# Optimization experiments

Hardware: AMD Instinct MI355X
Metric: run time of the kernel (lower is better)

Reference implementation:

```python
import jax, jax.numpy as jnp
import numpy as np

B, N, M = 262144, 8, 4  # batch, state dim, measurement dim


def _tril_square(x, n):
    """x: (b, n(n+1)/2) linearized lower-tri elems -> L @ L.T, (b, n, n)."""
    i, j = np.tril_indices(n)
    L = jnp.zeros((x.shape[0], n, n), dtype=x.dtype).at[:, i, j].set(x)
    return jnp.einsum('bik,bjk->bij', L, L)


def setup_inputs() -> dict:
    key = jax.random.key(0)
    ks = jax.random.split(key, 7)
    measurement = jax.random.normal(ks[0], (B, M), dtype=jnp.float32)
    state = jax.random.normal(ks[1], (B, N), dtype=jnp.float32)
    # SPD state covariance: A A^T / n + I
    A = jax.random.normal(ks[2], (B, N, N), dtype=jnp.float32) * 0.3
    state_cov = jnp.einsum('bik,bjk->bij', A, A) / N + jnp.eye(N, dtype=jnp.float32)
    F = jnp.eye(N, dtype=jnp.float32) + 0.1 * jax.random.normal(ks[3], (B, N, N), dtype=jnp.float32)
    H = jax.random.normal(ks[4], (B, M, N), dtype=jnp.float32) * 0.5
    process_noise = jax.random.normal(ks[5], (B, N * (N + 1) // 2), dtype=jnp.float32) * 0.1
    measurement_noise = jax.random.normal(ks[6], (B, M * (M + 1) // 2), dtype=jnp.float32) * 0.3
    return {
        'measurement': measurement, 'state': state, 'state_cov': state_cov,
        'F': F, 'H': H,
        'process_noise': process_noise, 'measurement_noise': measurement_noise,
    }


def reference(measurement, state, state_cov, F, H, process_noise, measurement_noise):
    b, n = state.shape
    m = measurement.shape[1]
    Q = _tril_square(process_noise, n)       # (b, n, n) process noise cov
    R = _tril_square(measurement_noise, m)   # (b, m, m) measurement noise cov

    # Predict
    new_state = jnp.einsum('bij,bj->bi', F, state)
    new_state_cov = jnp.einsum('bij,bjk,blk->bil', F, state_cov, F) + Q

    # Update
    prediction = jnp.einsum('bij,bj->bi', H, new_state)
    res = measurement - prediction
    res_cov = jnp.einsum('bij,bjk,blk->bil', H, new_state_cov, H) + R  # (b, m, m)
    PHt = jnp.einsum('bij,bkj->bik', new_state_cov, H)                 # (b, n, m)
    kgain = jnp.matmul(PHt, jnp.linalg.inv(res_cov))                   # (b, n, m)

    upd_state = new_state + jnp.einsum('bij,bj->bi', kgain, res)
    I = jnp.eye(n, dtype=state.dtype)
    upd_cov = jnp.matmul(I - jnp.matmul(kgain, H), new_state_cov)
    return prediction, upd_state, upd_cov
```

## Files before the change

kernel.cpp:

```cpp
#include <hip/hip_runtime.h>

#define DEVINL __device__ __forceinline__

#define TIX(i, j) ((i) * ((i) + 1) / 2 + (j))
#define SYM(arr, i, j) ((i) >= (j) ? arr[TIX(i, j)] : arr[TIX(j, i)])

DEVINL void inv4(const float* m, float* inv) {
    float s0 = m[0] * m[5] - m[1] * m[4];
    float s1 = m[0] * m[6] - m[2] * m[4];
    float s2 = m[0] * m[7] - m[3] * m[4];
    float s3 = m[1] * m[6] - m[2] * m[5];
    float s4 = m[1] * m[7] - m[3] * m[5];
    float s5 = m[2] * m[7] - m[3] * m[6];
    float c5 = m[10] * m[15] - m[11] * m[14];
    float c4 = m[9] * m[15] - m[11] * m[13];
    float c3 = m[9] * m[14] - m[10] * m[13];
    float c2 = m[8] * m[15] - m[11] * m[12];
    float c1 = m[8] * m[14] - m[10] * m[12];
    float c0 = m[8] * m[13] - m[9] * m[12];
    float det = s0 * c5 - s1 * c4 + s2 * c3 + s3 * c2 - s4 * c1 + s5 * c0;
    float id = 1.0f / det;
    inv[0]  = ( m[5] * c5 - m[6] * c4 + m[7] * c3) * id;
    inv[1]  = (-m[1] * c5 + m[2] * c4 - m[3] * c3) * id;
    inv[2]  = ( m[13] * s5 - m[14] * s4 + m[15] * s3) * id;
    inv[3]  = (-m[9] * s5 + m[10] * s4 - m[11] * s3) * id;
    inv[4]  = (-m[4] * c5 + m[6] * c2 - m[7] * c1) * id;
    inv[5]  = ( m[0] * c5 - m[2] * c2 + m[3] * c1) * id;
    inv[6]  = (-m[12] * s5 + m[14] * s2 - m[15] * s1) * id;
    inv[7]  = ( m[8] * s5 - m[10] * s2 + m[11] * s1) * id;
    inv[8]  = ( m[4] * c4 - m[5] * c2 + m[7] * c0) * id;
    inv[9]  = (-m[0] * c4 + m[1] * c2 - m[3] * c0) * id;
    inv[10] = ( m[12] * s4 - m[13] * s2 + m[15] * s0) * id;
    inv[11] = (-m[8] * s4 + m[9] * s2 - m[11] * s0) * id;
    inv[12] = (-m[4] * c3 + m[5] * c1 - m[6] * c0) * id;
    inv[13] = ( m[0] * c3 - m[1] * c1 + m[2] * c0) * id;
    inv[14] = (-m[12] * s3 + m[13] * s1 - m[14] * s0) * id;
    inv[15] = ( m[8] * s3 - m[9] * s1 + m[10] * s0) * id;
}

__global__ __launch_bounds__(256) void ekf_kernel(
    const float* __restrict__ meas,
    const float* __restrict__ state,
    const float* __restrict__ Pin,
    const float* __restrict__ Fin,
    const float* __restrict__ Hin,
    const float* __restrict__ pnin,
    const float* __restrict__ mnin,
    float* __restrict__ out_pred,
    float* __restrict__ out_state,
    float* __restrict__ out_cov)
{
    const int t  = threadIdx.x;
    const int bb = blockIdx.x * 256;
    const int b  = bb + t;

    __shared__ float4 buf[2304];

    {
        const float4* g = reinterpret_cast<const float4*>(pnin) + (size_t)bb * 9;
        #pragma unroll
        for (int i = 0; i < 9; ++i) buf[i * 256 + t] = g[i * 256 + t];
    }
    __syncthreads();
    float Pn[36];
    {
        float Lq[36];
        #pragma unroll
        for (int q = 0; q < 9; ++q) {
            float4 v = buf[t * 9 + q];
            Lq[4 * q] = v.x; Lq[4 * q + 1] = v.y; Lq[4 * q + 2] = v.z; Lq[4 * q + 3] = v.w;
        }
        #pragma unroll
        for (int i = 0; i < 8; ++i)
            #pragma unroll
            for (int j = 0; j <= i; ++j) {
                float acc = 0.f;
                #pragma unroll
                for (int k = 0; k <= j; ++k)
                    acc += Lq[TIX(i, k)] * Lq[TIX(j, k)];
                Pn[TIX(i, j)] = acc;
            }
    }
    __syncthreads();

    {
        const float4* g = reinterpret_cast<const float4*>(state) + (size_t)bb * 2;
        #pragma unroll
        for (int i = 0; i < 2; ++i) {
            int f = i * 256 + t;
            buf[(f >> 1) * 3 + (f & 1)] = g[f];
        }
    }
    __syncthreads();
    float s[8];
    {
        float4 a = buf[t * 3 + 0], c = buf[t * 3 + 1];
        s[0] = a.x; s[1] = a.y; s[2] = a.z; s[3] = a.w;
        s[4] = c.x; s[5] = c.y; s[6] = c.z; s[7] = c.w;
    }
    __syncthreads();

    float Ps[36];
    #pragma unroll
    for (int h = 0; h < 2; ++h) {
        {
            const float4* g = reinterpret_cast<const float4*>(Pin) + (size_t)bb * 16;
            #pragma unroll
            for (int i = 0; i < 8; ++i) {
                int fl = i * 256 + t;
                int bq = fl >> 3, q = fl & 7;
                buf[bq * 9 + q] = g[bq * 16 + 8 * h + q];
            }
        }
        __syncthreads();
        #pragma unroll
        for (int q = 0; q < 8; ++q) {
            float4 v = buf[t * 9 + q];
            const int row = 4 * h + (q >> 1), c0 = 4 * (q & 1);
            if (c0 + 0 <= row) Ps[TIX(row, c0 + 0)] = v.x;
            if (c0 + 1 <= row) Ps[TIX(row, c0 + 1)] = v.y;
            if (c0 + 2 <= row) Ps[TIX(row, c0 + 2)] = v.z;
            if (c0 + 3 <= row) Ps[TIX(row, c0 + 3)] = v.w;
        }
        __syncthreads();
    }

    float Fm[64];
    #pragma unroll
    for (int h = 0; h < 2; ++h) {
        {
            const float4* g = reinterpret_cast<const float4*>(Fin) + (size_t)bb * 16;
            #pragma unroll
            for (int i = 0; i < 8; ++i) {
                int fl = i * 256 + t;
                int bq = fl >> 3, q = fl & 7;
                buf[bq * 9 + q] = g[bq * 16 + 8 * h + q];
            }
        }
        __syncthreads();
        #pragma unroll
        for (int q = 0; q < 8; ++q) {
            float4 v = buf[t * 9 + q];
            Fm[32 * h + 4 * q + 0] = v.x;
            Fm[32 * h + 4 * q + 1] = v.y;
            Fm[32 * h + 4 * q + 2] = v.z;
            Fm[32 * h + 4 * q + 3] = v.w;
        }
        __syncthreads();
    }

    float ns[8];
    #pragma unroll
    for (int i = 0; i < 8; ++i) {
        float acc = 0.f;
        #pragma unroll
        for (int j = 0; j < 8; ++j) acc += Fm[i * 8 + j] * s[j];
        ns[i] = acc;
    }
    #pragma unroll
    for (int l = 0; l < 8; ++l) {
        float gcol[8];
        #pragma unroll
        for (int j = 0; j < 8; ++j) {
            float acc = 0.f;
            #pragma unroll
            for (int k = 0; k < 8; ++k) acc += SYM(Ps, j, k) * Fm[l * 8 + k];
            gcol[j] = acc;
        }
        #pragma unroll
        for (int i = l; i < 8; ++i) {
            float acc = Pn[TIX(i, l)];
            #pragma unroll
            for (int j = 0; j < 8; ++j) acc += Fm[i * 8 + j] * gcol[j];
            Pn[TIX(i, l)] = acc;
        }
    }

    float Hm[32];
    {
        const float4* g = reinterpret_cast<const float4*>(Hin) + (size_t)bb * 8;
        #pragma unroll
        for (int i = 0; i < 8; ++i) {
            int fl = i * 256 + t;
            buf[(fl >> 3) * 9 + (fl & 7)] = g[fl];
        }
    }
    __syncthreads();
    #pragma unroll
    for (int q = 0; q < 8; ++q) {
        float4 v = buf[t * 9 + q];
        Hm[4 * q + 0] = v.x; Hm[4 * q + 1] = v.y;
        Hm[4 * q + 2] = v.z; Hm[4 * q + 3] = v.w;
    }
    __syncthreads();

    float Rs[10];
    {
        const float2* g = reinterpret_cast<const float2*>(mnin) + (size_t)bb * 5;
        float2* buf2 = reinterpret_cast<float2*>(buf);
        #pragma unroll
        for (int i = 0; i < 5; ++i) buf2[i * 256 + t] = g[i * 256 + t];
    }
    __syncthreads();
    {
        const float2* buf2 = reinterpret_cast<const float2*>(buf);
        float Lr[10];
        #pragma unroll
        for (int p = 0; p < 5; ++p) {
            float2 v = buf2[t * 5 + p];
            Lr[2 * p] = v.x; Lr[2 * p + 1] = v.y;
        }
        #pragma unroll
        for (int i = 0; i < 4; ++i)
            #pragma unroll
            for (int j = 0; j <= i; ++j) {
                float acc = 0.f;
                #pragma unroll
                for (int k = 0; k <= j; ++k)
                    acc += Lr[TIX(i, k)] * Lr[TIX(j, k)];
                Rs[TIX(i, j)] = acc;
            }
    }
    __syncthreads();

    float pred[4], res[4], HP[32], Si[16], K[32], us[8];
    {
        float4 z = *(reinterpret_cast<const float4*>(meas) + b);
        const float zz[4] = {z.x, z.y, z.z, z.w};
        #pragma unroll
        for (int i = 0; i < 4; ++i) {
            float acc = 0.f;
            #pragma unroll
            for (int j = 0; j < 8; ++j) acc += Hm[i * 8 + j] * ns[j];
            pred[i] = acc;
            res[i] = zz[i] - acc;
        }

        #pragma unroll
        for (int i = 0; i < 4; ++i)
            #pragma unroll
            for (int k = 0; k < 8; ++k) {
                float acc = 0.f;
                #pragma unroll
                for (int j = 0; j < 8; ++j) acc += Hm[i * 8 + j] * SYM(Pn, j, k);
                HP[i * 8 + k] = acc;
            }

        float Sf[16];
        #pragma unroll
        for (int i = 0; i < 4; ++i)
            #pragma unroll
            for (int l = 0; l < 4; ++l) {
                float acc = SYM(Rs, i, l);
                #pragma unroll
                for (int k = 0; k < 8; ++k) acc += HP[i * 8 + k] * Hm[l * 8 + k];
                Sf[i * 4 + l] = acc;
            }
        inv4(Sf, Si);

        #pragma unroll
        for (int i = 0; i < 8; ++i)
            #pragma unroll
            for (int j = 0; j < 4; ++j) {
                float acc = 0.f;
                #pragma unroll
                for (int k = 0; k < 4; ++k) acc += HP[k * 8 + i] * Si[k * 4 + j];
                K[i * 4 + j] = acc;
            }

        *(reinterpret_cast<float4*>(out_pred) + b) =
            make_float4(pred[0], pred[1], pred[2], pred[3]);

        #pragma unroll
        for (int i = 0; i < 8; ++i) {
            float acc = ns[i];
            #pragma unroll
            for (int j = 0; j < 4; ++j) acc += K[i * 4 + j] * res[j];
            us[i] = acc;
        }
    }

    __syncthreads();
    buf[t * 3 + 0] = make_float4(us[0], us[1], us[2], us[3]);
    buf[t * 3 + 1] = make_float4(us[4], us[5], us[6], us[7]);
    __syncthreads();
    {
        float4* g = reinterpret_cast<float4*>(out_state) + (size_t)bb * 2;
        #pragma unroll
        for (int i = 0; i < 2; ++i) {
            int f = i * 256 + t;
            g[f] = buf[(f >> 1) * 3 + (f & 1)];
        }
    }
    __syncthreads();

    #pragma unroll
    for (int h = 0; h < 2; ++h) {
        #pragma unroll
        for (int r = 0; r < 4; ++r) {
            const int i = 4 * h + r;
            float Arow[8];
            #pragma unroll
            for (int j = 0; j < 8; ++j) {
                float acc = (i == j) ? 1.f : 0.f;
                #pragma unroll
                for (int k = 0; k < 4; ++k) acc -= K[i * 4 + k] * Hm[k * 8 + j];
                Arow[j] = acc;
            }
            float orow[8];
            #pragma unroll
            for (int j = 0; j < 8; ++j) {
                float acc = 0.f;
                #pragma unroll
                for (int k = 0; k < 8; ++k) acc += Arow[k] * SYM(Pn, k, j);
                orow[j] = acc;
            }
            buf[t * 9 + 2 * r + 0] = make_float4(orow[0], orow[1], orow[2], orow[3]);
            buf[t * 9 + 2 * r + 1] = make_float4(orow[4], orow[5], orow[6], orow[7]);
        }
        __syncthreads();
        {
            float4* g = reinterpret_cast<float4*>(out_cov) + (size_t)bb * 16;
            #pragma unroll
            for (int i = 0; i < 8; ++i) {
                int fl = i * 256 + t;
                int bq = fl >> 3, q = fl & 7;
                g[bq * 16 + 8 * h + q] = buf[bq * 9 + q];
            }
        }
        __syncthreads();
    }
}

extern "C" void kernel_launch(void* const* d_in, const int* in_sizes, int n_in,
                              void* d_out, int out_size, void* d_ws, size_t ws_size,
                              hipStream_t stream) {
    const float* meas  = (const float*)d_in[0];
    const float* state = (const float*)d_in[1];
    const float* Pin   = (const float*)d_in[2];
    const float* Fin   = (const float*)d_in[3];
    const float* Hin   = (const float*)d_in[4];
    const float* pn    = (const float*)d_in[5];
    const float* mn    = (const float*)d_in[6];

    const int B = in_sizes[1] / 8;

    float* out = (float*)d_out;
    float* out_pred  = out;
    float* out_state = out + (size_t)B * 4;
    float* out_cov   = out + (size_t)B * 12;

    dim3 block(256);
    dim3 grid(B / 256);
    ekf_kernel<<<grid, block, 0, stream>>>(meas, state, Pin, Fin, Hin, pn, mn,
                                           out_pred, out_state, out_cov);
}
```

Before: 261.7 us.

## Load inputs directly per thread and use symmetric Joseph-free covariance update

Input loads for state, P, F, H and noise factors now go straight from global memory per thread (strided float4 reads) instead of staging through shared memory with many barriers. The F P F^T product is split into two halves of F to lower peak register use, and only the lower triangle is computed. The update now forms P - HP^T S^-1 HP symmetrically and computes the state update via S^-1 res, avoiding explicit K and the (I-KH)P product. Uncoalesced per-thread loads may hurt memory efficiency, and the symmetric form can differ numerically from the reference's non-symmetric result.

Result: no change. 265.1 us (+1.3%).

```diff
diff --git a/kernel.cpp b/kernel.cpp
--- a/kernel.cpp
+++ b/kernel.cpp
@@ -56,159 +56,153 @@
 
     __shared__ float4 buf[2304];
 
-    {
-        const float4* g = reinterpret_cast<const float4*>(pnin) + (size_t)bb * 9;
-        #pragma unroll
-        for (int i = 0; i < 9; ++i) buf[i * 256 + t] = g[i * 256 + t];
-    }
-    __syncthreads();
-    float Pn[36];
-    {
-        float Lq[36];
-        #pragma unroll
-        for (int q = 0; q < 9; ++q) {
-            float4 v = buf[t * 9 + q];
-            Lq[4 * q] = v.x; Lq[4 * q + 1] = v.y; Lq[4 * q + 2] = v.z; Lq[4 * q + 3] = v.w;
-        }
-        #pragma unroll
-        for (int i = 0; i < 8; ++i)
-            #pragma unroll
-            for (int j = 0; j <= i; ++j) {
-                float acc = 0.f;
-                #pragma unroll
-                for (int k = 0; k <= j; ++k)
-                    acc += Lq[TIX(i, k)] * Lq[TIX(j, k)];
-                Pn[TIX(i, j)] = acc;
-            }
-    }
-    __syncthreads();
-
-    {
-        const float4* g = reinterpret_cast<const float4*>(state) + (size_t)bb * 2;
-        #pragma unroll
-        for (int i = 0; i < 2; ++i) {
-            int f = i * 256 + t;
-            buf[(f >> 1) * 3 + (f & 1)] = g[f];
-        }
-    }
-    __syncthreads();
     float s[8];
     {
-        float4 a = buf[t * 3 + 0], c = buf[t * 3 + 1];
+        const float4* g = reinterpret_cast<const float4*>(state) + (size_t)b * 2;
+        float4 a = g[0], c = g[1];
         s[0] = a.x; s[1] = a.y; s[2] = a.z; s[3] = a.w;
         s[4] = c.x; s[5] = c.y; s[6] = c.z; s[7] = c.w;
     }
-    __syncthreads();
 
     float Ps[36];
-    #pragma unroll
-    for (int h = 0; h < 2; ++h) {
-        {
-            const float4* g = reinterpret_cast<const float4*>(Pin) + (size_t)bb * 16;
-            #pragma unroll
-            for (int i = 0; i < 8; ++i) {
-                int fl = i * 256 + t;
-                int bq = fl >> 3, q = fl & 7;
-                buf[bq * 9 + q] = g[bq * 16 + 8 * h + q];
-            }
-        }
-        __syncthreads();
-        #pragma unroll
-        for (int q = 0; q < 8; ++q) {
-            float4 v = buf[t * 9 + q];
-            const int row = 4 * h + (q >> 1), c0 = 4 * (q & 1);
+    {
+        const float4* g = reinterpret_cast<const float4*>(Pin) + (size_t)b * 16;
+        #pragma unroll
+        for (int i = 0; i < 16; ++i) {
+            float4 v = g[i];
+            const int row = i / 2, c0 = (i % 2) * 4;
             if (c0 + 0 <= row) Ps[TIX(row, c0 + 0)] = v.x;
             if (c0 + 1 <= row) Ps[TIX(row, c0 + 1)] = v.y;
             if (c0 + 2 <= row) Ps[TIX(row, c0 + 2)] = v.z;
             if (c0 + 3 <= row) Ps[TIX(row, c0 + 3)] = v.w;
         }
-        __syncthreads();
-    }
-
-    float Fm[64];
-    #pragma unroll
-    for (int h = 0; h < 2; ++h) {
+    }
+
+    float Pn[36];
+    float ns[8];
+    float Ta[32];
+
+    {
+        float Fh[32];
         {
-            const float4* g = reinterpret_cast<const float4*>(Fin) + (size_t)bb * 16;
+            const float4* g = reinterpret_cast<const float4*>(Fin) + (size_t)b * 16;
             #pragma unroll
             for (int i = 0; i < 8; ++i) {
-                int fl = i * 256 + t;
-                int bq = fl >> 3, q = fl & 7;
-                buf[bq * 9 + q] = g[bq * 16 + 8 * h + q];
-            }
-        }
-        __syncthreads();
-        #pragma unroll
-        for (int q = 0; q < 8; ++q) {
-            float4 v = buf[t * 9 + q];
-            Fm[32 * h + 4 * q + 0] = v.x;
-            Fm[32 * h + 4 * q + 1] = v.y;
-            Fm[32 * h + 4 * q + 2] = v.z;
-            Fm[32 * h + 4 * q + 3] = v.w;
-        }
-        __syncthreads();
-    }
-
-    float ns[8];
-    #pragma unroll
-    for (int i = 0; i < 8; ++i) {
-        float acc = 0.f;
-        #pragma unroll
-        for (int j = 0; j < 8; ++j) acc += Fm[i * 8 + j] * s[j];
-        ns[i] = acc;
-    }
-    #pragma unroll
-    for (int l = 0; l < 8; ++l) {
-        float gcol[8];
-        #pragma unroll
-        for (int j = 0; j < 8; ++j) {
-            float acc = 0.f;
-            #pragma unroll
-            for (int k = 0; k < 8; ++k) acc += SYM(Ps, j, k) * Fm[l * 8 + k];
-            gcol[j] = acc;
-        }
-        #pragma unroll
-        for (int i = l; i < 8; ++i) {
-            float acc = Pn[TIX(i, l)];
-            #pragma unroll
-            for (int j = 0; j < 8; ++j) acc += Fm[i * 8 + j] * gcol[j];
-            Pn[TIX(i, l)] = acc;
-        }
+                float4 v = g[i];
+                Fh[4 * i] = v.x; Fh[4 * i + 1] = v.y; Fh[4 * i + 2] = v.z; Fh[4 * i + 3] = v.w;
+            }
+        }
+        #pragma unroll
+        for (int i = 0; i < 4; ++i) {
+            float acc = 0.f;
+            #pragma unroll
+            for (int j = 0; j < 8; ++j) acc += Fh[i * 8 + j] * s[j];
+            ns[i] = acc;
+        }
+        #pragma unroll
+        for (int l = 0; l < 4; ++l)
+            #pragma unroll
+            for (int j = 0; j < 8; ++j) {
+                float acc = 0.f;
+                #pragma unroll
+                for (int k = 0; k < 8; ++k) acc += SYM(Ps, j, k) * Fh[l * 8 + k];
+                Ta[l * 8 + j] = acc;
+            }
+        #pragma unroll
+        for (int i = 0; i < 4; ++i)
+            #pragma unroll
+            for (int l = 0; l <= i; ++l) {
+                float acc = 0.f;
+                #pragma unroll
+                for (int j = 0; j < 8; ++j) acc += Fh[i * 8 + j] * Ta[l * 8 + j];
+                Pn[TIX(i, l)] = acc;
+            }
+    }
+
+    {
+        float Fh[32];
+        {
+            const float4* g = reinterpret_cast<const float4*>(Fin) + (size_t)b * 16;
+            #pragma unroll
+            for (int i = 0; i < 8; ++i) {
+                float4 v = g[8 + i];
+                Fh[4 * i] = v.x; Fh[4 * i + 1] = v.y; Fh[4 * i + 2] = v.z; Fh[4 * i + 3] = v.w;
+            }
+        }
+        #pragma unroll
+        for (int r = 0; r < 4; ++r) {
+            float acc = 0.f;
+            #pragma unroll
+            for (int j = 0; j < 8; ++j) acc += Fh[r * 8 + j] * s[j];
+            ns[4 + r] = acc;
+        }
+        #pragma unroll
+        for (int r = 0; r < 4; ++r)
+            #pragma unroll
+            for (int l = 0; l < 4; ++l) {
+                float acc = 0.f;
+                #pragma unroll
+                for (int j = 0; j < 8; ++j) acc += Fh[r * 8 + j] * Ta[l * 8 + j];
+                Pn[TIX(4 + r, l)] = acc;
+            }
+        float Tb[32];
+        #pragma unroll
+        for (int r = 0; r < 4; ++r)
+            #pragma unroll
+            for (int j = 0; j < 8; ++j) {
+                float acc = 0.f;
+                #pragma unroll
+                for (int k = 0; k < 8; ++k) acc += SYM(Ps, j, k) * Fh[r * 8 + k];
+                Tb[r * 8 + j] = acc;
+            }
+        #pragma unroll
+        for (int r = 0; r < 4; ++r)
+            #pragma unroll
+            for (int q = 0; q <= r; ++q) {
+                float acc = 0.f;
+                #pragma unroll
+                for (int j = 0; j < 8; ++j) acc += Fh[r * 8 + j] * Tb[q * 8 + j];
+                Pn[TIX(4 + r, 4 + q)] = acc;
+            }
+    }
+
+    {
+        float Lq[36];
+        const float4* g = reinterpret_cast<const float4*>(pnin) + (size_t)b * 9;
+        #pragma unroll
+        for (int i = 0; i < 9; ++i) {
+            float4 v = g[i];
+            Lq[4 * i] = v.x; Lq[4 * i + 1] = v.y; Lq[4 * i + 2] = v.z; Lq[4 * i + 3] = v.w;
+        }
+        #pragma unroll
+        for (int i = 0; i < 8; ++i)
+            #pragma unroll
+            for (int j = 0; j <= i; ++j) {
+                float acc = Pn[TIX(i, j)];
+                #pragma unroll
+                for (int k = 0; k <= j; ++k)
+                    acc += Lq[TIX(i, k)] * Lq[TIX(j, k)];
+                Pn[TIX(i, j)] = acc;
+            }
     }
 
     float Hm[32];
     {
-        const float4* g = reinterpret_cast<const float4*>(Hin) + (size_t)bb * 8;
+        const float4* g = reinterpret_cast<const float4*>(Hin) + (size_t)b * 8;
         #pragma unroll
         for (int i = 0; i < 8; ++i) {
-            int fl = i * 256 + t;
-            buf[(fl >> 3) * 9 + (fl & 7)] = g[fl];
-        }
-    }
-    __syncthreads();
-    #pragma unroll
-    for (int q = 0; q < 8; ++q) {
-        float4 v = buf[t * 9 + q];
-        Hm[4 * q + 0] = v.x; Hm[4 * q + 1] = v.y;
-        Hm[4 * q + 2] = v.z; Hm[4 * q + 3] = v.w;
-    }
-    __syncthreads();
-
+            float4 v = g[i];
+            Hm[4 * i] = v.x; Hm[4 * i + 1] = v.y; Hm[4 * i + 2] = v.z; Hm[4 * i + 3] = v.w;
+        }
+    }
     float Rs[10];
     {
-        const float2* g = reinterpret_cast<const float2*>(mnin) + (size_t)bb * 5;
-        float2* buf2 = reinterpret_cast<float2*>(buf);
-        #pragma unroll
-        for (int i = 0; i < 5; ++i) buf2[i * 256 + t] = g[i * 256 + t];
-    }
-    __syncthreads();
-    {
-        const float2* buf2 = reinterpret_cast<const float2*>(buf);
         float Lr[10];
-        #pragma unroll
-        for (int p = 0; p < 5; ++p) {
-            float2 v = buf2[t * 5 + p];
-            Lr[2 * p] = v.x; Lr[2 * p + 1] = v.y;
+        const float2* g = reinterpret_cast<const float2*>(mnin) + (size_t)b * 5;
+        #pragma unroll
+        for (int i = 0; i < 5; ++i) {
+            float2 v = g[i];
+            Lr[2 * i] = v.x; Lr[2 * i + 1] = v.y;
         }
         #pragma unroll
         for (int i = 0; i < 4; ++i)
@@ -221,9 +215,8 @@
                 Rs[TIX(i, j)] = acc;
             }
     }
-    __syncthreads();
-
-    float pred[4], res[4], HP[32], Si[16], K[32], us[8];
+
+    float res[4];
     {
         float4 z = *(reinterpret_cast<const float4*>(meas) + b);
         const float zz[4] = {z.x, z.y, z.z, z.w};
@@ -232,55 +225,62 @@
             float acc = 0.f;
             #pragma unroll
             for (int j = 0; j < 8; ++j) acc += Hm[i * 8 + j] * ns[j];
-            pred[i] = acc;
             res[i] = zz[i] - acc;
-        }
-
+            if (i == 3) {
+                float4 pv;
+                pv.x = zz[0] - res[0]; pv.y = zz[1] - res[1];
+                pv.z = zz[2] - res[2]; pv.w = zz[3] - res[3];
+                *(reinterpret_cast<float4*>(out_pred) + b) = pv;
+            }
+        }
+    }
+
+    float HP[32];
+    #pragma unroll
+    for (int i = 0; i < 4; ++i)
+        #pragma unroll
+        for (int k = 0; k < 8; ++k) {
+            float acc = 0.f;
+            #pragma unroll
+            for (int j = 0; j < 8; ++j) acc += Hm[i * 8 + j] * SYM(Pn, j, k);
+            HP[i * 8 + k] = acc;
+        }
+
+    float Si[16];
+    {
+        float Sf[16];
         #pragma unroll
         for (int i = 0; i < 4; ++i)
             #pragma unroll
-            for (int k = 0; k < 8; ++k) {
-                float acc = 0.f;
-                #pragma unroll
-                for (int j = 0; j < 8; ++j) acc += Hm[i * 8 + j] * SYM(Pn, j, k);
-                HP[i * 8 + k] = acc;
-            }
-
-        float Sf[16];
-        #pragma unroll
-        for (int i = 0; i < 4; ++i)
-            #pragma unroll
-            for (int l = 0; l < 4; ++l) {
+            for (int l = 0; l <= i; ++l) {
                 float acc = SYM(Rs, i, l);
                 #pragma unroll
                 for (int k = 0; k < 8; ++k) acc += HP[i * 8 + k] * Hm[l * 8 + k];
                 Sf[i * 4 + l] = acc;
+                Sf[l * 4 + i] = acc;
             }
         inv4(Sf, Si);
-
-        #pragma unroll
-        for (int i = 0; i < 8; ++i)
-            #pragma unroll
-            for (int j = 0; j < 4; ++j) {
-                float acc = 0.f;
-                #pragma unroll
-                for (int k = 0; k < 4; ++k) acc += HP[k * 8 + i] * Si[k * 4 + j];
-                K[i * 4 + j] = acc;
-            }
-
-        *(reinterpret_cast<float4*>(out_pred) + b) =
-            make_float4(pred[0], pred[1], pred[2], pred[3]);
-
+    }
+
+    float us[8];
+    {
+        float w[4];
+        #pragma unroll
+        for (int a = 0; a < 4; ++a) {
+            float acc = 0.f;
+            #pragma unroll
+            for (int c = 0; c < 4; ++c) acc += Si[a * 4 + c] * res[c];
+            w[a] = acc;
+        }
         #pragma unroll
         for (int i = 0; i < 8; ++i) {
             float acc = ns[i];
             #pragma unroll
-            for (int j = 0; j < 4; ++j) acc += K[i * 4 + j] * res[j];
+            for (int a = 0; a < 4; ++a) acc += HP[a * 8 + i] * w[a];
             us[i] = acc;
         }
     }
 
-    __syncthreads();
     buf[t * 3 + 0] = make_float4(us[0], us[1], us[2], us[3]);
     buf[t * 3 + 1] = make_float4(us[4], us[5], us[6], us[7]);
     __syncthreads();
@@ -294,29 +294,37 @@
     }
     __syncthreads();
 
+    {
+        float M[32];
+        #pragma unroll
+        for (int a = 0; a < 4; ++a)
+            #pragma unroll
+            for (int j = 0; j < 8; ++j) {
+                float acc = 0.f;
+                #pragma unroll
+                for (int c = 0; c < 4; ++c) acc += Si[a * 4 + c] * HP[c * 8 + j];
+                M[a * 8 + j] = acc;
+            }
+        #pragma unroll
+        for (int i = 0; i < 8; ++i)
+            #pragma unroll
+            for (int l = 0; l <= i; ++l) {
+                float acc = Pn[TIX(i, l)];
+                #pragma unroll
+                for (int a = 0; a < 4; ++a) acc -= HP[a * 8 + i] * M[a * 8 + l];
+                Pn[TIX(i, l)] = acc;
+            }
+    }
+
     #pragma unroll
     for (int h = 0; h < 2; ++h) {
         #pragma unroll
         for (int r = 0; r < 4; ++r) {
             const int i = 4 * h + r;
-            float Arow[8];
-            #pragma unroll
-            for (int j = 0; j < 8; ++j) {
-                float acc = (i == j) ? 1.f : 0.f;
-                #pragma unroll
-                for (int k = 0; k < 4; ++k) acc -= K[i * 4 + k] * Hm[k * 8 + j];
-                Arow[j] = acc;
-            }
-            float orow[8];
-            #pragma unroll
-            for (int j = 0; j < 8; ++j) {
-                float acc = 0.f;
-                #pragma unroll
-                for (int k = 0; k < 8; ++k) acc += Arow[k] * SYM(Pn, k, j);
-                orow[j] = acc;
-            }
-            buf[t * 9 + 2 * r + 0] = make_float4(orow[0], orow[1], orow[2], orow[3]);
-            buf[t * 9 + 2 * r + 1] = make_float4(orow[4], orow[5], orow[6], orow[7]);
+            buf[t * 9 + 2 * r + 0] = make_float4(SYM(Pn, i, 0), SYM(Pn, i, 1),
+                                                 SYM(Pn, i, 2), SYM(Pn, i, 3));
+            buf[t * 9 + 2 * r + 1] = make_float4(SYM(Pn, i, 4), SYM(Pn, i, 5),
+                                                 SYM(Pn, i, 6), SYM(Pn, i, 7));
         }
         __syncthreads();
         {
```

## Use single-wavefront blocks, drop barriers, and compute covariance update via symmetric Joseph-free form

Applied to the files above, without the earlier changes.

Shrinks blocks to 64 threads (one wavefront) so several __syncthreads can be removed and shared memory per block drops. Reformulates the update: the Kalman gain is never formed explicitly; the state update uses HP^T (S^-1 res), and the covariance update computes P - HP^T S^-1 HP on the lower triangle only. It also builds S symmetrically and adds R in place. Removing barriers within a single wavefront depends on lockstep execution, and the symmetric-form covariance changes rounding compared with (I-KH)P.

New measurement: 256.0 us. 2.2% less time.

```diff
diff --git a/kernel.cpp b/kernel.cpp
--- a/kernel.cpp
+++ b/kernel.cpp
@@ -38,7 +38,7 @@
     inv[15] = ( m[8] * s3 - m[9] * s1 + m[10] * s0) * id;
 }
 
-__global__ __launch_bounds__(256) void ekf_kernel(
+__global__ __launch_bounds__(64) void ekf_kernel(
     const float* __restrict__ meas,
     const float* __restrict__ state,
     const float* __restrict__ Pin,
@@ -51,15 +51,15 @@
     float* __restrict__ out_cov)
 {
     const int t  = threadIdx.x;
-    const int bb = blockIdx.x * 256;
+    const int bb = blockIdx.x * 64;
     const int b  = bb + t;
 
-    __shared__ float4 buf[2304];
+    __shared__ float4 buf[576];
 
     {
         const float4* g = reinterpret_cast<const float4*>(pnin) + (size_t)bb * 9;
         #pragma unroll
-        for (int i = 0; i < 9; ++i) buf[i * 256 + t] = g[i * 256 + t];
+        for (int i = 0; i < 9; ++i) buf[i * 64 + t] = g[i * 64 + t];
     }
     __syncthreads();
     float Pn[36];
@@ -81,13 +81,12 @@
                 Pn[TIX(i, j)] = acc;
             }
     }
-    __syncthreads();
 
     {
         const float4* g = reinterpret_cast<const float4*>(state) + (size_t)bb * 2;
         #pragma unroll
         for (int i = 0; i < 2; ++i) {
-            int f = i * 256 + t;
+            int f = i * 64 + t;
             buf[(f >> 1) * 3 + (f & 1)] = g[f];
         }
     }
@@ -98,7 +97,6 @@
         s[0] = a.x; s[1] = a.y; s[2] = a.z; s[3] = a.w;
         s[4] = c.x; s[5] = c.y; s[6] = c.z; s[7] = c.w;
     }
-    __syncthreads();
 
     float Ps[36];
     #pragma unroll
@@ -107,7 +105,7 @@
             const float4* g = reinterpret_cast<const float4*>(Pin) + (size_t)bb * 16;
             #pragma unroll
             for (int i = 0; i < 8; ++i) {
-                int fl = i * 256 + t;
+                int fl = i * 64 + t;
                 int bq = fl >> 3, q = fl & 7;
                 buf[bq * 9 + q] = g[bq * 16 + 8 * h + q];
             }
@@ -132,7 +130,7 @@
             const float4* g = reinterpret_cast<const float4*>(Fin) + (size_t)bb * 16;
             #pragma unroll
             for (int i = 0; i < 8; ++i) {
-                int fl = i * 256 + t;
+                int fl = i * 64 + t;
                 int bq = fl >> 3, q = fl & 7;
                 buf[bq * 9 + q] = g[bq * 16 + 8 * h + q];
             }
@@ -181,7 +179,7 @@
         const float4* g = reinterpret_cast<const float4*>(Hin) + (size_t)bb * 8;
         #pragma unroll
         for (int i = 0; i < 8; ++i) {
-            int fl = i * 256 + t;
+            int fl = i * 64 + t;
             buf[(fl >> 3) * 9 + (fl & 7)] = g[fl];
         }
     }
@@ -192,16 +190,55 @@
         Hm[4 * q + 0] = v.x; Hm[4 * q + 1] = v.y;
         Hm[4 * q + 2] = v.z; Hm[4 * q + 3] = v.w;
     }
-    __syncthreads();
-
-    float Rs[10];
+
+    float res[4];
+    {
+        float4 z = *(reinterpret_cast<const float4*>(meas) + b);
+        float pr[4];
+        #pragma unroll
+        for (int i = 0; i < 4; ++i) {
+            float acc = 0.f;
+            #pragma unroll
+            for (int j = 0; j < 8; ++j) acc += Hm[i * 8 + j] * ns[j];
+            pr[i] = acc;
+        }
+        res[0] = z.x - pr[0]; res[1] = z.y - pr[1];
+        res[2] = z.z - pr[2]; res[3] = z.w - pr[3];
+        *(reinterpret_cast<float4*>(out_pred) + b) =
+            make_float4(pr[0], pr[1], pr[2], pr[3]);
+    }
+
+    float HP[32];
+    #pragma unroll
+    for (int i = 0; i < 4; ++i)
+        #pragma unroll
+        for (int k = 0; k < 8; ++k) {
+            float acc = 0.f;
+            #pragma unroll
+            for (int j = 0; j < 8; ++j) acc += Hm[i * 8 + j] * SYM(Pn, j, k);
+            HP[i * 8 + k] = acc;
+        }
+
+    float Sf[16];
+    #pragma unroll
+    for (int i = 0; i < 4; ++i)
+        #pragma unroll
+        for (int l = 0; l <= i; ++l) {
+            float acc = 0.f;
+            #pragma unroll
+            for (int k = 0; k < 8; ++k) acc += HP[i * 8 + k] * Hm[l * 8 + k];
+            Sf[i * 4 + l] = acc;
+            Sf[l * 4 + i] = acc;
+        }
+
     {
         const float2* g = reinterpret_cast<const float2*>(mnin) + (size_t)bb * 5;
         float2* buf2 = reinterpret_cast<float2*>(buf);
         #pragma unroll
-        for (int i = 0; i < 5; ++i) buf2[i * 256 + t] = g[i * 256 + t];
-    }
-    __syncthreads();
+        for (int i = 0; i < 5; ++i) buf2[i * 64 + t] = g[i * 64 + t];
+    }
+    __syncthreads();
+    float Si[16];
     {
         const float2* buf2 = reinterpret_cast<const float2*>(buf);
         float Lr[10];
@@ -218,69 +255,31 @@
                 #pragma unroll
                 for (int k = 0; k <= j; ++k)
                     acc += Lr[TIX(i, k)] * Lr[TIX(j, k)];
-                Rs[TIX(i, j)] = acc;
-            }
-    }
-    __syncthreads();
-
-    float pred[4], res[4], HP[32], Si[16], K[32], us[8];
-    {
-        float4 z = *(reinterpret_cast<const float4*>(meas) + b);
-        const float zz[4] = {z.x, z.y, z.z, z.w};
-        #pragma unroll
-        for (int i = 0; i < 4; ++i) {
-            float acc = 0.f;
-            #pragma unroll
-            for (int j = 0; j < 8; ++j) acc += Hm[i * 8 + j] * ns[j];
-            pred[i] = acc;
-            res[i] = zz[i] - acc;
-        }
-
-        #pragma unroll
-        for (int i = 0; i < 4; ++i)
-            #pragma unroll
-            for (int k = 0; k < 8; ++k) {
-                float acc = 0.f;
-                #pragma unroll
-                for (int j = 0; j < 8; ++j) acc += Hm[i * 8 + j] * SYM(Pn, j, k);
-                HP[i * 8 + k] = acc;
-            }
-
-        float Sf[16];
-        #pragma unroll
-        for (int i = 0; i < 4; ++i)
-            #pragma unroll
-            for (int l = 0; l < 4; ++l) {
-                float acc = SYM(Rs, i, l);
-                #pragma unroll
-                for (int k = 0; k < 8; ++k) acc += HP[i * 8 + k] * Hm[l * 8 + k];
-                Sf[i * 4 + l] = acc;
+                Sf[i * 4 + j] += acc;
+                if (i != j) Sf[j * 4 + i] += acc;
             }
         inv4(Sf, Si);
-
-        #pragma unroll
-        for (int i = 0; i < 8; ++i)
-            #pragma unroll
-            for (int j = 0; j < 4; ++j) {
-                float acc = 0.f;
-                #pragma unroll
-                for (int k = 0; k < 4; ++k) acc += HP[k * 8 + i] * Si[k * 4 + j];
-                K[i * 4 + j] = acc;
-            }
-
-        *(reinterpret_cast<float4*>(out_pred) + b) =
-            make_float4(pred[0], pred[1], pred[2], pred[3]);
-
+    }
+
+    float us[8];
+    {
+        float w[4];
+        #pragma unroll
+        for (int a = 0; a < 4; ++a) {
+            float acc = 0.f;
+            #pragma unroll
+            for (int c = 0; c < 4; ++c) acc += Si[a * 4 + c] * res[c];
+            w[a] = acc;
+        }
         #pragma unroll
         for (int i = 0; i < 8; ++i) {
             float acc = ns[i];
             #pragma unroll
-            for (int j = 0; j < 4; ++j) acc += K[i * 4 + j] * res[j];
+            for (int a = 0; a < 4; ++a) acc += HP[a * 8 + i] * w[a];
             us[i] = acc;
         }
     }
 
-    __syncthreads();
     buf[t * 3 + 0] = make_float4(us[0], us[1], us[2], us[3]);
     buf[t * 3 + 1] = make_float4(us[4], us[5], us[6], us[7]);
     __syncthreads();
@@ -288,42 +287,49 @@
         float4* g = reinterpret_cast<float4*>(out_state) + (size_t)bb * 2;
         #pragma unroll
         for (int i = 0; i < 2; ++i) {
-            int f = i * 256 + t;
+            int f = i * 64 + t;
             g[f] = buf[(f >> 1) * 3 + (f & 1)];
         }
     }
-    __syncthreads();
-
-    #pragma unroll
-    for (int h = 0; h < 2; ++h) {
-        #pragma unroll
-        for (int r = 0; r < 4; ++r) {
-            const int i = 4 * h + r;
-            float Arow[8];
-            #pragma unroll
-            for (int j = 0; j < 8; ++j) {
-                float acc = (i == j) ? 1.f : 0.f;
-                #pragma unroll
-                for (int k = 0; k < 4; ++k) acc -= K[i * 4 + k] * Hm[k * 8 + j];
-                Arow[j] = acc;
-            }
-            float orow[8];
+
+    {
+        float M[32];
+        #pragma unroll
+        for (int a = 0; a < 4; ++a)
             #pragma unroll
             for (int j = 0; j < 8; ++j) {
                 float acc = 0.f;
                 #pragma unroll
-                for (int k = 0; k < 8; ++k) acc += Arow[k] * SYM(Pn, k, j);
-                orow[j] = acc;
-            }
-            buf[t * 9 + 2 * r + 0] = make_float4(orow[0], orow[1], orow[2], orow[3]);
-            buf[t * 9 + 2 * r + 1] = make_float4(orow[4], orow[5], orow[6], orow[7]);
+                for (int c = 0; c < 4; ++c) acc += Si[a * 4 + c] * HP[c * 8 + j];
+                M[a * 8 + j] = acc;
+            }
+        #pragma unroll
+        for (int i = 0; i < 8; ++i)
+            #pragma unroll
+            for (int l = 0; l <= i; ++l) {
+                float acc = Pn[TIX(i, l)];
+                #pragma unroll
+                for (int a = 0; a < 4; ++a) acc -= HP[a * 8 + i] * M[a * 8 + l];
+                Pn[TIX(i, l)] = acc;
+            }
+    }
+
+    #pragma unroll
+    for (int h = 0; h < 2; ++h) {
+        #pragma unroll
+        for (int r = 0; r < 4; ++r) {
+            const int i = 4 * h + r;
+            buf[t * 9 + 2 * r + 0] = make_float4(SYM(Pn, i, 0), SYM(Pn, i, 1),
+                                                 SYM(Pn, i, 2), SYM(Pn, i, 3));
+            buf[t * 9 + 2 * r + 1] = make_float4(SYM(Pn, i, 4), SYM(Pn, i, 5),
+                                                 SYM(Pn, i, 6), SYM(Pn, i, 7));
         }
         __syncthreads();
         {
             float4* g = reinterpret_cast<float4*>(out_cov) + (size_t)bb * 16;
             #pragma unroll
             for (int i = 0; i < 8; ++i) {
-                int fl = i * 256 + t;
+                int fl = i * 64 + t;
                 int bq = fl >> 3, q = fl & 7;
                 g[bq * 16 + 8 * h + q] = buf[bq * 9 + q];
             }
@@ -350,8 +356,8 @@
     float* out_state = out + (size_t)B * 4;
     float* out_cov   = out + (size_t)B * 12;
 
-    dim3 block(256);
-    dim3 grid(B / 256);
+    dim3 block(64);
+    dim3 grid(B / 64);
     ekf_kernel<<<grid, block, 0, stream>>>(meas, state, Pin, Fin, Hin, pn, mn,
                                            out_pred, out_state, out_cov);
 }
```
